# Kernel tuning notes

Hardware: AMD Instinct MI355X
Metric: run time of the kernel (lower is better)

Reference implementation:

```python
import jax, jax.numpy as jnp
import numpy as np

VOCAB = 100000
EMB = 128
D = 8
K = 128
SUB = EMB // D  # 16
BN_EPS = 1e-3  # keras BatchNormalization default epsilon


def setup_inputs() -> dict:
    key = jax.random.key(0)
    k1, k2, k3 = jax.random.split(key, 3)
    ids = jax.random.randint(k1, (1024, 128), 0, VOCAB, dtype=jnp.int64)
    query_wemb = jax.random.normal(k2, (VOCAB, EMB), dtype=jnp.float32)
    centroids = jax.random.normal(k3, (D, K, SUB), dtype=jnp.float32)
    return {"ids": ids, "query_wemb": query_wemb, "centroids": centroids}


def reference(ids, query_wemb, centroids):
    d, k, sub = centroids.shape
    emb = d * sub
    flat = ids.reshape(-1)                      # [N]
    x = query_wemb[flat].reshape(-1, d, sub)    # [N, d, sub]

    norm_x = jnp.sum(x * x, axis=-1, keepdims=True)          # [N, d, 1]
    norm_c = jnp.sum(centroids * centroids, axis=-1)[None]   # [1, d, k]
    dot = jnp.einsum('nds,dks->ndk', x, centroids)           # [N, d, k]
    response = -norm_x + 2.0 * dot - norm_c                  # [N, d, k]

    # BatchNorm(scale=False, center=False), training=True: batch stats over
    # axes (0,1), per-k channel (keras default axis=-1)
    mean = jnp.mean(response, axis=(0, 1), keepdims=True)
    var = jnp.var(response, axis=(0, 1), keepdims=True)
    resp_bn = (response - mean) * jax.lax.rsqrt(var + BN_EPS)

    codes = jnp.argmax(resp_bn, axis=-1)                     # [N, d]

    # per-subspace centroid gather (non-shared centroids)
    outputs = centroids[jnp.arange(d)[None, :], codes]       # [N, d, sub]

    # straight-through estimator
    out_st = x + jax.lax.stop_gradient(outputs - x)          # [N, d, sub]
    return out_st.reshape(ids.shape + (emb,))
```

## Files before the change

kernel.cpp:

```cpp
#include <hip/hip_runtime.h>


constexpr int NTOK = 131072;
constexpr int ST   = 2320;
constexpr float EPS = 0.001f;


__global__ __launch_bounds__(256) void k1_stats(const int* __restrict__ ids,
                                                const float* __restrict__ wemb,
                                                float* __restrict__ partials,
                                                int tpb)
{
    __shared__ float xs[32][132];
    __shared__ float nrm[32][8];
    const int t = threadIdx.x;
    const int b = blockIdx.x;

    float g[4][4];
#pragma unroll
    for (int i = 0; i < 4; ++i)
#pragma unroll
        for (int j = 0; j < 4; ++j) g[i][j] = 0.f;
    float sx = 0.f, hh = 0.f, s2 = 0.f;

    const int d_g = t >> 4;
    const int r0  = ((t >> 2) & 3) << 2;
    const int c0  = (t & 3) << 2;
    const int u   = t & 127;
    const int d_s = u >> 4;
    const int s_s = u & 15;

    const int nchunks = tpb >> 5;
    for (int ch = 0; ch < nchunks; ++ch) {
        const int n0 = b * tpb + ch * 32;
#pragma unroll
        for (int rep = 0; rep < 4; ++rep) {
            int i = t + rep * 256;
            int n = i >> 5, f = i & 31;
            int id = ids[n0 + n];
            float4 v = *(const float4*)(wemb + (size_t)id * 128 + f * 4);
            *(float4*)(&xs[n][f * 4]) = v;
        }
        __syncthreads();
        {
            int n = t >> 3, dd = t & 7;
            const float* xp = &xs[n][dd * 16];
            float4 a = *(const float4*)(xp);
            float4 bq = *(const float4*)(xp + 4);
            float4 c = *(const float4*)(xp + 8);
            float4 dq = *(const float4*)(xp + 12);
            float acc = a.x*a.x + a.y*a.y + a.z*a.z + a.w*a.w;
            acc += bq.x*bq.x + bq.y*bq.y + bq.z*bq.z + bq.w*bq.w;
            acc += c.x*c.x + c.y*c.y + c.z*c.z + c.w*c.w;
            acc += dq.x*dq.x + dq.y*dq.y + dq.z*dq.z + dq.w*dq.w;
            nrm[n][dd] = acc;
        }
        __syncthreads();
        if (t < 128) {
            for (int n = 0; n < 32; ++n) {
                const float* xp = &xs[n][d_g * 16];
                float4 av = *(const float4*)(xp + r0);
                float4 bv = *(const float4*)(xp + c0);
                float aa[4] = {av.x, av.y, av.z, av.w};
                float bb[4] = {bv.x, bv.y, bv.z, bv.w};
#pragma unroll
                for (int i = 0; i < 4; ++i)
#pragma unroll
                    for (int j = 0; j < 4; ++j)
                        g[i][j] = fmaf(aa[i], bb[j], g[i][j]);
            }
        } else {
            for (int n = 0; n < 32; ++n) {
                float xv = xs[n][d_s * 16 + s_s];
                float nv = nrm[n][d_s];
                sx += xv;
                hh = fmaf(nv, xv, hh);
                if (s_s == 0) s2 = fmaf(nv, nv, s2);
            }
        }
        __syncthreads();
    }
    float* pb = partials + (size_t)b * ST;
    if (t < 128) {
        const int base = d_g * 256;
#pragma unroll
        for (int i = 0; i < 4; ++i)
#pragma unroll
            for (int j = 0; j < 4; ++j)
                pb[base + (r0 + i) * 16 + (c0 + j)] = g[i][j];
    } else {
        pb[2048 + d_s * 16 + s_s] = sx;
        pb[2176 + d_s * 16 + s_s] = hh;
        if (s_s == 0) pb[2304 + d_s] = s2;
    }
}

__global__ __launch_bounds__(256) void k2a_reduce(float* __restrict__ partials, int nb)
{
    const int idx = blockIdx.x * 256 + threadIdx.x;
    if (idx >= 2312) return;
    const int y = blockIdx.y;
    float acc[8] = {0.f, 0.f, 0.f, 0.f, 0.f, 0.f, 0.f, 0.f};
    int b = y;
    while (b + 7 * 32 < nb) {
#pragma unroll
        for (int u = 0; u < 8; ++u)
            acc[u] += partials[(size_t)(b + u * 32) * ST + idx];
        b += 8 * 32;
    }
    while (b < nb) { acc[0] += partials[(size_t)b * ST + idx]; b += 32; }
    float s = ((acc[0] + acc[1]) + (acc[2] + acc[3]))
            + ((acc[4] + acc[5]) + (acc[6] + acc[7]));
    partials[(size_t)y * ST + idx] = s;
}

__global__ __launch_bounds__(256) void k2b_reduce(const float* __restrict__ partials,
                                                  float* __restrict__ stats)
{
    const int idx = blockIdx.x * 256 + threadIdx.x;
    if (idx >= 2312) return;
    float acc[8] = {0.f, 0.f, 0.f, 0.f, 0.f, 0.f, 0.f, 0.f};
#pragma unroll
    for (int j = 0; j < 4; ++j)
#pragma unroll
        for (int u = 0; u < 8; ++u)
            acc[u] += partials[(size_t)(j * 8 + u) * ST + idx];
    stats[idx] = ((acc[0] + acc[1]) + (acc[2] + acc[3]))
               + ((acc[4] + acc[5]) + (acc[6] + acc[7]));
}

__global__ __launch_bounds__(128) void k3_final(const float* __restrict__ stats,
                                                const float* __restrict__ centroids,
                                                float2* __restrict__ ab)
{
    __shared__ float st[2312];
    const int t = threadIdx.x;
    for (int i = t; i < 2312; i += 128) st[i] = stats[i];
    __syncthreads();
    const int k = t;

    double Sn[8], Sn_tot = 0.0, S2_tot = 0.0;
#pragma unroll
    for (int d = 0; d < 8; ++d) {
        double s = 0.0;
        for (int ss = 0; ss < 16; ++ss) s += (double)st[d * 256 + ss * 17];
        Sn[d] = s; Sn_tot += s;
        S2_tot += (double)st[2304 + d];
    }
    double sr = -Sn_tot, sr2 = S2_tot;
    double ncd[8];
    for (int d = 0; d < 8; ++d) {
        const float* cp = centroids + d * 2048 + k * 16;
        float cv[16];
#pragma unroll
        for (int s = 0; s < 16; ++s) cv[s] = cp[s];
        double nc = 0, cdSx = 0, ch = 0, cGc = 0;
        for (int s = 0; s < 16; ++s) {
            nc   += (double)cv[s] * cv[s];
            cdSx += (double)cv[s] * st[2048 + d * 16 + s];
            ch   += (double)cv[s] * st[2176 + d * 16 + s];
            double rd = 0;
            for (int s2i = 0; s2i < 16; ++s2i)
                rd += (double)st[d * 256 + s * 16 + s2i] * cv[s2i];
            cGc += (double)cv[s] * rd;
        }
        ncd[d] = nc;
        sr  += 2.0 * cdSx - (double)NTOK * nc;
        sr2 += 4.0 * cGc + (double)NTOK * nc * nc + 2.0 * nc * Sn[d]
               - 4.0 * ch - 4.0 * nc * cdSx;
    }
    const double M = (double)NTOK * 8.0;
    double mean = sr / M;
    double var  = sr2 / M - mean * mean;
    float alpha = (float)(1.0 / sqrt(var + (double)EPS));
#pragma unroll
    for (int d = 0; d < 8; ++d) {
        float beta = (float)((double)alpha * (-ncd[d] - mean));
        ab[d * 128 + k] = make_float2(2.f * alpha, beta);
    }
}

__global__ __launch_bounds__(256) void k4_main(const int* __restrict__ ids,
                                               const float* __restrict__ wemb,
                                               const float* __restrict__ centroids,
                                               const float2* __restrict__ ab,
                                               float* __restrict__ out)
{
    __shared__ float cs[128][16];
    __shared__ float2 gb_s[128];
    const int t = threadIdx.x;
    const int d = blockIdx.y;
    const float* cd = centroids + d * 2048;
#pragma unroll
    for (int i = 0; i < 2; ++i)
        ((float4*)cs)[t + i * 256] = ((const float4*)cd)[t + i * 256];
    if (t < 128) gb_s[t] = ab[d * 128 + t];
    __syncthreads();

    const int n0 = blockIdx.x * 1024 + t;
    float x[4][16];
    float nx2[4], best[4];
    int code[4];
#pragma unroll
    for (int j = 0; j < 4; ++j) {
        const int n = n0 + j * 256;
        const float* xp = wemb + (size_t)ids[n] * 128 + d * 16;
        float4 v0 = *(const float4*)(xp);
        float4 v1 = *(const float4*)(xp + 4);
        float4 v2 = *(const float4*)(xp + 8);
        float4 v3 = *(const float4*)(xp + 12);
        x[j][0] = v0.x; x[j][1] = v0.y; x[j][2]  = v0.z; x[j][3]  = v0.w;
        x[j][4] = v1.x; x[j][5] = v1.y; x[j][6]  = v1.z; x[j][7]  = v1.w;
        x[j][8] = v2.x; x[j][9] = v2.y; x[j][10] = v2.z; x[j][11] = v2.w;
        x[j][12] = v3.x; x[j][13] = v3.y; x[j][14] = v3.z; x[j][15] = v3.w;
        float s = 0.f;
#pragma unroll
        for (int q = 0; q < 16; ++q) s = fmaf(x[j][q], x[j][q], s);
        nx2[j] = -0.5f * s;
        best[j] = -3.4e38f;
        code[j] = 0;
    }
#pragma unroll 2
    for (int k = 0; k < 128; ++k) {
        float2 gb = gb_s[k];
        float4 c0 = *(const float4*)(&cs[k][0]);
        float4 c1 = *(const float4*)(&cs[k][4]);
        float4 c2 = *(const float4*)(&cs[k][8]);
        float4 c3 = *(const float4*)(&cs[k][12]);
        float c[16] = {c0.x, c0.y, c0.z, c0.w, c1.x, c1.y, c1.z, c1.w,
                       c2.x, c2.y, c2.z, c2.w, c3.x, c3.y, c3.z, c3.w};
#pragma unroll
        for (int j = 0; j < 4; ++j) {
            float acc = nx2[j];
#pragma unroll
            for (int s = 0; s < 16; ++s) acc = fmaf(c[s], x[j][s], acc);
            float score = fmaf(gb.x, acc, gb.y);
            bool p = score > best[j];
            best[j] = p ? score : best[j];
            code[j] = p ? k : code[j];
        }
    }
#pragma unroll
    for (int j = 0; j < 4; ++j) {
        const int n = n0 + j * 256;
        const float* cw = cd + code[j] * 16;
        float* op = out + (size_t)n * 128 + d * 16;
#pragma unroll
        for (int s = 0; s < 16; s += 4) {
            float4 cv = *(const float4*)(cw + s);
            float4 o;
            o.x = x[j][s + 0] + (cv.x - x[j][s + 0]);
            o.y = x[j][s + 1] + (cv.y - x[j][s + 1]);
            o.z = x[j][s + 2] + (cv.z - x[j][s + 2]);
            o.w = x[j][s + 3] + (cv.w - x[j][s + 3]);
            *(float4*)(op + s) = o;
        }
    }
}

extern "C" void kernel_launch(void* const* d_in, const int* in_sizes, int n_in,
                              void* d_out, int out_size, void* d_ws, size_t ws_size,
                              hipStream_t stream)
{
    const int* ids    = (const int*)d_in[0];
    const float* wemb = (const float*)d_in[1];
    const float* cent = (const float*)d_in[2];
    float* out = (float*)d_out;
    float* ws  = (float*)d_ws;

    int p1b = 512;
    if (ws_size < ((size_t)512 * ST + 2320 + 2048) * 4) p1b = 256;
    if (ws_size < ((size_t)256 * ST + 2320 + 2048) * 4) p1b = 128;
    const int tpb = NTOK / p1b;

    float* partials = ws;
    float* stats    = ws + (size_t)p1b * ST;
    float2* ab      = (float2*)(stats + 2320);

    hipLaunchKernelGGL(k1_stats,   dim3(p1b),     dim3(256), 0, stream, ids, wemb, partials, tpb);
    hipLaunchKernelGGL(k2a_reduce, dim3(10, 32),  dim3(256), 0, stream, partials, p1b);
    hipLaunchKernelGGL(k2b_reduce, dim3(10),      dim3(256), 0, stream, partials, stats);
    hipLaunchKernelGGL(k3_final,   dim3(1),       dim3(128), 0, stream, stats, cent, ab);
    hipLaunchKernelGGL(k4_main,    dim3(128, 8),  dim3(256), 0, stream, ids, wemb, cent, ab, out);
}
```

Measured before the change: 126.3 us.

## Process one token per thread in main kernel and read centroids via uniform loads

The main kernel now handles one token per thread instead of four. It drops the shared-memory centroid staging and the barrier, reading centroids and BN coefficients directly from global memory as block-uniform (scalar/cached) loads, and sets launch bounds of 8 blocks per CU. The grid grows from 128 to 512 blocks per subspace to raise occupancy and hide gather latency. The stats pass also uses more partial blocks when the workspace allows. The trade-off is losing the four-way reuse of each centroid load across tokens, and each block is now much shorter.

New measurement: 140.1 us. 11.0% more time.

```diff
diff --git a/kernel.cpp b/kernel.cpp
--- a/kernel.cpp
+++ b/kernel.cpp
@@ -180,81 +180,61 @@
     }
 }
 
-__global__ __launch_bounds__(256) void k4_main(const int* __restrict__ ids,
-                                               const float* __restrict__ wemb,
-                                               const float* __restrict__ centroids,
-                                               const float2* __restrict__ ab,
-                                               float* __restrict__ out)
-{
-    __shared__ float cs[128][16];
-    __shared__ float2 gb_s[128];
+__global__ __launch_bounds__(256, 8) void k4_main(const int* __restrict__ ids,
+                                                  const float* __restrict__ wemb,
+                                                  const float* __restrict__ centroids,
+                                                  const float2* __restrict__ ab,
+                                                  float* __restrict__ out)
+{
     const int t = threadIdx.x;
     const int d = blockIdx.y;
+    const int n = blockIdx.x * 256 + t;
     const float* cd = centroids + d * 2048;
-#pragma unroll
-    for (int i = 0; i < 2; ++i)
-        ((float4*)cs)[t + i * 256] = ((const float4*)cd)[t + i * 256];
-    if (t < 128) gb_s[t] = ab[d * 128 + t];
-    __syncthreads();
-
-    const int n0 = blockIdx.x * 1024 + t;
-    float x[4][16];
-    float nx2[4], best[4];
-    int code[4];
-#pragma unroll
-    for (int j = 0; j < 4; ++j) {
-        const int n = n0 + j * 256;
-        const float* xp = wemb + (size_t)ids[n] * 128 + d * 16;
+    const float2* gb = ab + (size_t)d * 128;
+
+    const float* xp = wemb + (size_t)ids[n] * 128 + d * 16;
+    float x[16];
+    {
         float4 v0 = *(const float4*)(xp);
         float4 v1 = *(const float4*)(xp + 4);
         float4 v2 = *(const float4*)(xp + 8);
         float4 v3 = *(const float4*)(xp + 12);
-        x[j][0] = v0.x; x[j][1] = v0.y; x[j][2]  = v0.z; x[j][3]  = v0.w;
-        x[j][4] = v1.x; x[j][5] = v1.y; x[j][6]  = v1.z; x[j][7]  = v1.w;
-        x[j][8] = v2.x; x[j][9] = v2.y; x[j][10] = v2.z; x[j][11] = v2.w;
-        x[j][12] = v3.x; x[j][13] = v3.y; x[j][14] = v3.z; x[j][15] = v3.w;
-        float s = 0.f;
-#pragma unroll
-        for (int q = 0; q < 16; ++q) s = fmaf(x[j][q], x[j][q], s);
-        nx2[j] = -0.5f * s;
-        best[j] = -3.4e38f;
-        code[j] = 0;
-    }
-#pragma unroll 2
+        x[0] = v0.x; x[1] = v0.y; x[2]  = v0.z; x[3]  = v0.w;
+        x[4] = v1.x; x[5] = v1.y; x[6]  = v1.z; x[7]  = v1.w;
+        x[8] = v2.x; x[9] = v2.y; x[10] = v2.z; x[11] = v2.w;
+        x[12] = v3.x; x[13] = v3.y; x[14] = v3.z; x[15] = v3.w;
+    }
+    float s = 0.f;
+#pragma unroll
+    for (int q = 0; q < 16; ++q) s = fmaf(x[q], x[q], s);
+    const float nx2 = -0.5f * s;
+    float best = -3.4e38f;
+    int code = 0;
+
+#pragma unroll 4
     for (int k = 0; k < 128; ++k) {
-        float2 gb = gb_s[k];
-        float4 c0 = *(const float4*)(&cs[k][0]);
-        float4 c1 = *(const float4*)(&cs[k][4]);
-        float4 c2 = *(const float4*)(&cs[k][8]);
-        float4 c3 = *(const float4*)(&cs[k][12]);
-        float c[16] = {c0.x, c0.y, c0.z, c0.w, c1.x, c1.y, c1.z, c1.w,
-                       c2.x, c2.y, c2.z, c2.w, c3.x, c3.y, c3.z, c3.w};
-#pragma unroll
-        for (int j = 0; j < 4; ++j) {
-            float acc = nx2[j];
-#pragma unroll
-            for (int s = 0; s < 16; ++s) acc = fmaf(c[s], x[j][s], acc);
-            float score = fmaf(gb.x, acc, gb.y);
-            bool p = score > best[j];
-            best[j] = p ? score : best[j];
-            code[j] = p ? k : code[j];
-        }
-    }
-#pragma unroll
-    for (int j = 0; j < 4; ++j) {
-        const int n = n0 + j * 256;
-        const float* cw = cd + code[j] * 16;
-        float* op = out + (size_t)n * 128 + d * 16;
-#pragma unroll
-        for (int s = 0; s < 16; s += 4) {
-            float4 cv = *(const float4*)(cw + s);
-            float4 o;
-            o.x = x[j][s + 0] + (cv.x - x[j][s + 0]);
-            o.y = x[j][s + 1] + (cv.y - x[j][s + 1]);
-            o.z = x[j][s + 2] + (cv.z - x[j][s + 2]);
-            o.w = x[j][s + 3] + (cv.w - x[j][s + 3]);
-            *(float4*)(op + s) = o;
-        }
+        const float* cp = cd + k * 16;
+        float acc = nx2;
+#pragma unroll
+        for (int q = 0; q < 16; ++q) acc = fmaf(cp[q], x[q], acc);
+        float2 g = gb[k];
+        float score = fmaf(g.x, acc, g.y);
+        bool p = score > best;
+        best = p ? score : best;
+        code = p ? k : code;
+    }
+
+    const float* cw = cd + code * 16;
+    float* op = out + (size_t)n * 128 + d * 16;
+#pragma unroll
+    for (int q = 0; q < 16; q += 4) {
+        float4 cv = *(const float4*)(cw + q);
+        float4 o;
+        o.x = x[q + 0] + (cv.x - x[q + 0]);
+        o.y = x[q + 1] + (cv.y - x[q + 1]);
+        o.z = x[q + 2] + (cv.z - x[q + 2]);
+        o.w = x[q + 3] + (cv.w - x[q + 3]);
+        *(float4*)(op + q) = o;
     }
 }
 
@@ -268,9 +248,10 @@
     float* out = (float*)d_out;
     float* ws  = (float*)d_ws;
 
-    int p1b = 512;
-    if (ws_size < ((size_t)512 * ST + 2320 + 2048) * 4) p1b = 256;
-    if (ws_size < ((size_t)256 * ST + 2320 + 2048) * 4) p1b = 128;
+    int p1b = 1024;
+    if (ws_size < ((size_t)1024 * ST + 2320 + 2048) * 4) p1b = 512;
+    if (ws_size < ((size_t)512  * ST + 2320 + 2048) * 4) p1b = 256;
+    if (ws_size < ((size_t)256  * ST + 2320 + 2048) * 4) p1b = 128;
     const int tpb = NTOK / p1b;
 
     float* partials = ws;
@@ -281,5 +262,5 @@
     hipLaunchKernelGGL(k2a_reduce, dim3(10, 32),  dim3(256), 0, stream, partials, p1b);
     hipLaunchKernelGGL(k2b_reduce, dim3(10),      dim3(256), 0, stream, partials, stats);
     hipLaunchKernelGGL(k3_final,   dim3(1),       dim3(128), 0, stream, stats, cent, ab);
-    hipLaunchKernelGGL(k4_main,    dim3(128, 8),  dim3(256), 0, stream, ids, wemb, cent, ab, out);
-}
+    hipLaunchKernelGGL(k4_main,    dim3(512, 8),  dim3(256), 0, stream, ids, wemb, cent, ab, out);
+}
```
